# Performance work log

Hardware: AMD Instinct MI355X
Metric: run time of the kernel (lower is better)

Reference implementation:

```python
import jax, jax.numpy as jnp
import numpy as np

N_NODES = 50000
N_EDGES = 640000
DIM_IN = 128
DIM_OUT = 32
NUM_GRAPHS = 64


def setup_inputs() -> dict:
    key = jax.random.key(0)
    ks = jax.random.split(key, 8)
    x = jax.random.normal(ks[0], (N_NODES, DIM_IN), dtype=jnp.float32)
    edge_index = jax.random.randint(ks[1], (2, N_EDGES), 0, N_NODES, dtype=jnp.int64)
    batch = jnp.sort(jax.random.randint(ks[2], (N_NODES,), 0, NUM_GRAPHS, dtype=jnp.int64))
    s = 1.0 / np.sqrt(DIM_IN)
    W1 = jax.random.normal(ks[3], (DIM_IN, DIM_IN), dtype=jnp.float32) * s
    b1 = jnp.zeros((DIM_IN,), dtype=jnp.float32)
    W2 = jax.random.normal(ks[4], (DIM_IN, DIM_IN), dtype=jnp.float32) * s
    b2 = jnp.zeros((DIM_IN,), dtype=jnp.float32)
    Wh = jax.random.normal(ks[5], (DIM_IN, DIM_OUT), dtype=jnp.float32) * s
    bh = jnp.zeros((DIM_OUT,), dtype=jnp.float32)
    return {"x": x, "edge_index": edge_index, "batch": batch,
            "W1": W1, "b1": b1, "W2": W2, "b2": b2, "Wh": Wh, "bh": bh}


def _gcn_conv(x, src, dst, norm, W, b):
    # GCNConv: h = x @ W; out[i] = sum_{(j->i)} norm_e * h[j] + b
    h = x @ W
    msg = h[src] * norm[:, None]                      # [E+N, D] gather + scale
    out = jax.ops.segment_sum(msg, dst, num_segments=x.shape[0])
    return out + b


def reference(x, edge_index, batch, W1, b1, W2, b2, Wh, bh):
    n = x.shape[0]
    loops = jnp.arange(n, dtype=edge_index.dtype)
    src = jnp.concatenate([edge_index[0], loops])     # add self-loops
    dst = jnp.concatenate([edge_index[1], loops])
    # symmetric normalization: deg^{-1/2}[src] * deg^{-1/2}[dst]
    deg = jax.ops.segment_sum(jnp.ones_like(dst, dtype=x.dtype), dst, num_segments=n)
    dinv = jnp.where(deg > 0, jax.lax.rsqrt(deg), 0.0)
    norm = dinv[src] * dinv[dst]

    h = jax.nn.relu(_gcn_conv(x, src, dst, norm, W1, b1))   # dropout = identity (eval)
    h = jax.nn.relu(_gcn_conv(h, src, dst, norm, W2, b2))
    pooled = jax.ops.segment_sum(h, batch, num_segments=NUM_GRAPHS)  # global_add_pool
    logits = pooled @ Wh + bh
    return jax.nn.log_softmax(logits, axis=1)
```

## Files before the change

### kernel.cpp

```cpp
#include <hip/hip_runtime.h>
#include <hip/hip_bf16.h>
#include <math.h>

#define N_NODES 50000
#define N_EDGES 640000
#define DIM     128
#define NGRAPH  64
#define DOUT    32
#define CAP     64
#define LDSS 136
#define LDSF 132

#define G_GEMM  782
#define N_FILL  625
#define G_FRONT (G_GEMM + N_FILL)

#define G_PREP  209

typedef unsigned short u16;
typedef __attribute__((ext_vector_type(8))) short bf16x8;
typedef __attribute__((ext_vector_type(4))) float f32x4;

__device__ __forceinline__ u16 f2bf(float f) {
    unsigned u = __float_as_uint(f);
    return (u16)((u + 0x7FFFu + ((u >> 16) & 1u)) >> 16);
}
__device__ __forceinline__ float bf2f(u16 h) {
    return __uint_as_float(((unsigned)h) << 16);
}
__device__ __forceinline__ short2 cvt2(float x, float y) {
    __hip_bfloat162 h = __float22bfloat162_rn(make_float2(x, y));
    return *(short2*)&h;
}
__device__ __forceinline__ void upk(unsigned u, float& lo, float& hi) {
    lo = __uint_as_float(u << 16);
    hi = __uint_as_float(u & 0xFFFF0000u);
}

__global__ __launch_bounds__(256) void k_prep(const float* __restrict__ W1,
                                              const float* __restrict__ W2,
                                              u16* __restrict__ W1s,
                                              u16* __restrict__ W2s,
                                              float* __restrict__ pooled,
                                              int* __restrict__ cnt) {
    int b = blockIdx.x;
    int tid = threadIdx.x;
    if (b < 128) {
        int t = (b & 63) * 256 + tid;
        int j = t & 7, lane = (t >> 3) & 63, kc = (t >> 9) & 3, nt = t >> 11;
        int k = kc * 32 + (lane >> 4) * 8 + j;
        int n = nt * 16 + (lane & 15);
        if (b < 64) W1s[t] = f2bf(W1[k * 128 + n]);
        else        W2s[t] = f2bf(W2[k * 128 + n]);
    } else if (b < 160) {
        int t = (b - 128) * 256 + tid;
        pooled[t] = 0.f;
    } else {
        int t = (b - 160) * 256 + tid;
        if (t < 12500) {
            int4 z = {0, 0, 0, 0};
            *(int4*)(cnt + t * 4) = z;
        }
    }
}

__global__ __launch_bounds__(256) void k_front(const float* __restrict__ X,
                                               const int* __restrict__ src,
                                               const int* __restrict__ dst,
                                               int* __restrict__ cnt,
                                               int* __restrict__ bucket,
                                               const u16* __restrict__ Ws,
                                               u16* __restrict__ Y) {
    int b   = blockIdx.x;
    int tid = threadIdx.x;

    if (b < G_GEMM) {
        int wv   = tid >> 6;
        int lane = tid & 63;
        int row0 = b * 64 + wv * 16;
        int m    = lane & 15;
        int quad = lane >> 4;
        int ar = min(row0 + m, N_NODES - 1);
        const float* Arow = X + (size_t)ar * DIM;
        bf16x8 a[4];
#pragma unroll
        for (int kc = 0; kc < 4; ++kc) {
            const float4* p4 = (const float4*)(Arow + kc * 32 + quad * 8);
            float4 p = p4[0], q = p4[1];
            short2 s0 = cvt2(p.x, p.y), s1 = cvt2(p.z, p.w);
            short2 s2 = cvt2(q.x, q.y), s3 = cvt2(q.z, q.w);
            bf16x8 av;
            av[0] = s0.x; av[1] = s0.y; av[2] = s1.x; av[3] = s1.y;
            av[4] = s2.x; av[5] = s2.y; av[6] = s3.x; av[7] = s3.y;
            a[kc] = av;
        }
#pragma unroll
        for (int nt = 0; nt < 8; ++nt) {
            f32x4 acc = {0.f, 0.f, 0.f, 0.f};
#pragma unroll
            for (int kc = 0; kc < 4; ++kc) {
                bf16x8 bb = *(const bf16x8*)(Ws + ((size_t)(nt * 4 + kc) * 64 + lane) * 8);
                acc = __builtin_amdgcn_mfma_f32_16x16x32_bf16(a[kc], bb, acc, 0, 0, 0);
            }
            int col = nt * 16 + m;
#pragma unroll
            for (int r = 0; r < 4; ++r) {
                int rr = row0 + quad * 4 + r;
                if (rr < N_NODES) Y[(size_t)rr * DIM + col] = f2bf(acc[r]);
            }
        }
    } else {
        int e = (b - G_GEMM) * 1024 + tid * 4;
        int4 s4 = *(const int4*)(src + e);
        int4 d4 = *(const int4*)(dst + e);
        int p0 = atomicAdd(&cnt[d4.x], 1);
        int p1 = atomicAdd(&cnt[d4.y], 1);
        int p2 = atomicAdd(&cnt[d4.z], 1);
        int p3 = atomicAdd(&cnt[d4.w], 1);
        bucket[d4.x * CAP + p0] = s4.x;
        bucket[d4.y * CAP + p1] = s4.y;
        bucket[d4.z * CAP + p2] = s4.z;
        bucket[d4.w * CAP + p3] = s4.w;
    }
}

__global__ __launch_bounds__(256) void k_agg_gemm(const u16* __restrict__ H,
                                                  const int* __restrict__ bucket,
                                                  const int* __restrict__ cnt,
                                                  const float* __restrict__ bias,
                                                  const u16* __restrict__ Ws,
                                                  u16* __restrict__ Y) {
    __shared__ u16 As[16][LDSS];
    int tid    = threadIdx.x;
    int nloc   = tid >> 4;
    int lane16 = tid & 15;
    int node   = blockIdx.x * 16 + nloc;

    int deg = cnt[node];
    float dself = rsqrtf((float)(deg + 1));
    int e0 = node * CAP, e1 = e0 + deg;
    const uint4* H4 = (const uint4*)H;
    uint4 sv = H4[(size_t)node * 16 + lane16];
    float a0[8], a1[8] = {}, a2[8] = {}, a3[8] = {};
    {
        float lo, hi;
        upk(sv.x, lo, hi); a0[0] = dself * lo; a0[1] = dself * hi;
        upk(sv.y, lo, hi); a0[2] = dself * lo; a0[3] = dself * hi;
        upk(sv.z, lo, hi); a0[4] = dself * lo; a0[5] = dself * hi;
        upk(sv.w, lo, hi); a0[6] = dself * lo; a0[7] = dself * hi;
    }
    int4 c0, c1;
    if (e0 < e1) { c0 = *(const int4*)(bucket + e0); c1 = *(const int4*)(bucket + e0 + 4); }
    for (int e = e0; e < e1; e += 8) {
        int4 p0 = c0, p1 = c1;
        if (e + 8 < e1) {
            c0 = *(const int4*)(bucket + e + 8);
            c1 = *(const int4*)(bucket + e + 12);
        }
        int   idx[8];
        float w[8];
        uint4 v[8];
        int   cd[8];
        idx[0] = p0.x; idx[1] = p0.y; idx[2] = p0.z; idx[3] = p0.w;
        idx[4] = p1.x; idx[5] = p1.y; idx[6] = p1.z; idx[7] = p1.w;
#pragma unroll
        for (int u = 0; u < 8; ++u) {
            bool in = (e + u) < e1;
            w[u]   = in ? 1.f : 0.f;
            idx[u] = in ? idx[u] : 0;
        }
#pragma unroll
        for (int u = 0; u < 8; ++u) cd[u] = cnt[idx[u]];
#pragma unroll
        for (int u = 0; u < 8; ++u) v[u] = H4[(size_t)idx[u] * 16 + lane16];
#pragma unroll
        for (int u = 0; u < 8; ++u) w[u] *= rsqrtf((float)(cd[u] + 1));
#pragma unroll
        for (int u = 0; u < 8; ++u) {
            float* a = (u & 3) == 0 ? a0 : (u & 3) == 1 ? a1 : (u & 3) == 2 ? a2 : a3;
            float lo, hi;
            upk(v[u].x, lo, hi); a[0] = fmaf(w[u], lo, a[0]); a[1] = fmaf(w[u], hi, a[1]);
            upk(v[u].y, lo, hi); a[2] = fmaf(w[u], lo, a[2]); a[3] = fmaf(w[u], hi, a[3]);
            upk(v[u].z, lo, hi); a[4] = fmaf(w[u], lo, a[4]); a[5] = fmaf(w[u], hi, a[5]);
            upk(v[u].w, lo, hi); a[6] = fmaf(w[u], lo, a[6]); a[7] = fmaf(w[u], hi, a[7]);
        }
    }
    {
        float di = dself;
        const float4* b4 = (const float4*)bias;
        float4 blo = b4[lane16 * 2], bhi = b4[lane16 * 2 + 1];
        float r0 = fmaxf(di * (a0[0] + a1[0] + a2[0] + a3[0]) + blo.x, 0.f);
        float r1 = fmaxf(di * (a0[1] + a1[1] + a2[1] + a3[1]) + blo.y, 0.f);
        float r2 = fmaxf(di * (a0[2] + a1[2] + a2[2] + a3[2]) + blo.z, 0.f);
        float r3 = fmaxf(di * (a0[3] + a1[3] + a2[3] + a3[3]) + blo.w, 0.f);
        float r4 = fmaxf(di * (a0[4] + a1[4] + a2[4] + a3[4]) + bhi.x, 0.f);
        float r5 = fmaxf(di * (a0[5] + a1[5] + a2[5] + a3[5]) + bhi.y, 0.f);
        float r6 = fmaxf(di * (a0[6] + a1[6] + a2[6] + a3[6]) + bhi.z, 0.f);
        float r7 = fmaxf(di * (a0[7] + a1[7] + a2[7] + a3[7]) + bhi.w, 0.f);
        short2 s0 = cvt2(r0, r1), s1 = cvt2(r2, r3), s2 = cvt2(r4, r5), s3 = cvt2(r6, r7);
        uint4 o;
        o.x = *(unsigned*)&s0; o.y = *(unsigned*)&s1;
        o.z = *(unsigned*)&s2; o.w = *(unsigned*)&s3;
        *(uint4*)(&As[nloc][lane16 * 8]) = o;
    }
    __syncthreads();

    int wv   = tid >> 6;
    int lane = tid & 63;
    int m    = lane & 15;
    int quad = lane >> 4;
    bf16x8 a[4];
#pragma unroll
    for (int kc = 0; kc < 4; ++kc)
        a[kc] = *(const bf16x8*)(&As[m][kc * 32 + quad * 8]);
    float di[4];
#pragma unroll
    for (int r = 0; r < 4; ++r)
        di[r] = rsqrtf((float)(cnt[blockIdx.x * 16 + quad * 4 + r] + 1));
#pragma unroll
    for (int i = 0; i < 2; ++i) {
        int nt = wv * 2 + i;
        f32x4 acc = {0.f, 0.f, 0.f, 0.f};
#pragma unroll
        for (int kc = 0; kc < 4; ++kc) {
            bf16x8 b = *(const bf16x8*)(Ws + ((size_t)(nt * 4 + kc) * 64 + lane) * 8);
            acc = __builtin_amdgcn_mfma_f32_16x16x32_bf16(a[kc], b, acc, 0, 0, 0);
        }
        int col = nt * 16 + m;
#pragma unroll
        for (int r = 0; r < 4; ++r) {
            int rr = blockIdx.x * 16 + quad * 4 + r;
            Y[(size_t)rr * DIM + col] = f2bf(acc[r] * di[r]);
        }
    }
}

__global__ __launch_bounds__(256) void k_agg_pool(const u16* __restrict__ H,
                                                  const int* __restrict__ bucket,
                                                  const int* __restrict__ cnt,
                                                  const float* __restrict__ bias,
                                                  const int* __restrict__ batch,
                                                  float* __restrict__ pooled) {
    __shared__ float As[16][LDSF];
    __shared__ int bs[16];
    int tid  = threadIdx.x;
    int nloc = tid >> 4;
    int lane = tid & 15;
    int node = blockIdx.x * 16 + nloc;

    int deg = cnt[node];
    int e0 = node * CAP, e1 = e0 + deg;
    const uint4* H4 = (const uint4*)H;
    uint4 sv = H4[(size_t)node * 16 + lane];
    float a0[8], a1[8] = {}, a2[8] = {}, a3[8] = {};
    upk(sv.x, a0[0], a0[1]); upk(sv.y, a0[2], a0[3]);
    upk(sv.z, a0[4], a0[5]); upk(sv.w, a0[6], a0[7]);
    int4 c0, c1;
    if (e0 < e1) { c0 = *(const int4*)(bucket + e0); c1 = *(const int4*)(bucket + e0 + 4); }
    for (int e = e0; e < e1; e += 8) {
        int4 p0 = c0, p1 = c1;
        if (e + 8 < e1) {
            c0 = *(const int4*)(bucket + e + 8);
            c1 = *(const int4*)(bucket + e + 12);
        }
        int   idx[8];
        float w[8];
        uint4 v[8];
        idx[0] = p0.x; idx[1] = p0.y; idx[2] = p0.z; idx[3] = p0.w;
        idx[4] = p1.x; idx[5] = p1.y; idx[6] = p1.z; idx[7] = p1.w;
#pragma unroll
        for (int u = 0; u < 8; ++u) {
            bool in = (e + u) < e1;
            w[u]   = in ? 1.f : 0.f;
            idx[u] = in ? idx[u] : 0;
        }
#pragma unroll
        for (int u = 0; u < 8; ++u) v[u] = H4[(size_t)idx[u] * 16 + lane];
#pragma unroll
        for (int u = 0; u < 8; ++u) {
            float* a = (u & 3) == 0 ? a0 : (u & 3) == 1 ? a1 : (u & 3) == 2 ? a2 : a3;
            float lo, hi;
            upk(v[u].x, lo, hi); a[0] = fmaf(w[u], lo, a[0]); a[1] = fmaf(w[u], hi, a[1]);
            upk(v[u].y, lo, hi); a[2] = fmaf(w[u], lo, a[2]); a[3] = fmaf(w[u], hi, a[3]);
            upk(v[u].z, lo, hi); a[4] = fmaf(w[u], lo, a[4]); a[5] = fmaf(w[u], hi, a[5]);
            upk(v[u].w, lo, hi); a[6] = fmaf(w[u], lo, a[6]); a[7] = fmaf(w[u], hi, a[7]);
        }
    }
    {
        float di = rsqrtf((float)(deg + 1));
        const float4* b4 = (const float4*)bias;
        float4 blo = b4[lane * 2], bhi = b4[lane * 2 + 1];
        float4 olo, ohi;
        olo.x = fmaxf(di * (a0[0] + a1[0] + a2[0] + a3[0]) + blo.x, 0.f);
        olo.y = fmaxf(di * (a0[1] + a1[1] + a2[1] + a3[1]) + blo.y, 0.f);
        olo.z = fmaxf(di * (a0[2] + a1[2] + a2[2] + a3[2]) + blo.z, 0.f);
        olo.w = fmaxf(di * (a0[3] + a1[3] + a2[3] + a3[3]) + blo.w, 0.f);
        ohi.x = fmaxf(di * (a0[4] + a1[4] + a2[4] + a3[4]) + bhi.x, 0.f);
        ohi.y = fmaxf(di * (a0[5] + a1[5] + a2[5] + a3[5]) + bhi.y, 0.f);
        ohi.z = fmaxf(di * (a0[6] + a1[6] + a2[6] + a3[6]) + bhi.z, 0.f);
        ohi.w = fmaxf(di * (a0[7] + a1[7] + a2[7] + a3[7]) + bhi.w, 0.f);
        *(float4*)(&As[nloc][lane * 8])     = olo;
        *(float4*)(&As[nloc][lane * 8 + 4]) = ohi;
    }
    if (lane == 0) bs[nloc] = batch[node];
    __syncthreads();

    if (tid < 128) {
        float acc = 0.f;
        int cb = bs[0];
#pragma unroll
        for (int n = 0; n < 16; ++n) {
            int b = bs[n];
            if (b != cb) {
                atomicAdd(&pooled[cb * DIM + tid], acc);
                acc = 0.f; cb = b;
            }
            acc += As[n][tid];
        }
        atomicAdd(&pooled[cb * DIM + tid], acc);
    }
}

__global__ __launch_bounds__(64) void k_head(const float* __restrict__ pooled,
                                             const float* __restrict__ Wh,
                                             const float* __restrict__ bh,
                                             float* __restrict__ out) {
    int g = blockIdx.x;
    int lane = threadIdx.x;
    int c = lane & 31;
    const float* p = pooled + g * DIM;
    float lg = bh[c];
#pragma unroll 8
    for (int k = 0; k < DIM; ++k) lg = fmaf(p[k], Wh[k * DOUT + c], lg);
    float m = lg;
    for (int off = 16; off >= 1; off >>= 1) m = fmaxf(m, __shfl_xor(m, off, 32));
    float ex = expf(lg - m);
    float s = ex;
    for (int off = 16; off >= 1; off >>= 1) s += __shfl_xor(s, off, 32);
    if (lane < 32) out[g * DOUT + c] = lg - m - logf(s);
}

extern "C" void kernel_launch(void* const* d_in, const int* in_sizes, int n_in,
                              void* d_out, int out_size, void* d_ws, size_t ws_size,
                              hipStream_t stream) {
    const float* x     = (const float*)d_in[0];
    const int*   ei    = (const int*)d_in[1];
    const int*   batch = (const int*)d_in[2];
    const float* W1    = (const float*)d_in[3];
    const float* b1    = (const float*)d_in[4];
    const float* W2    = (const float*)d_in[5];
    const float* b2    = (const float*)d_in[6];
    const float* Wh    = (const float*)d_in[7];
    const float* bh    = (const float*)d_in[8];
    float* out = (float*)d_out;
    const int* src = ei;
    const int* dst = ei + N_EDGES;

    char* ws = (char*)d_ws;
    size_t off = 0;
    auto alloc = [&](size_t bytes) {
        void* p = ws + off;
        off += (bytes + 255) & ~(size_t)255;
        return p;
    };
    u16*   bufA   = (u16*) alloc((size_t)N_NODES * DIM * 2);
    u16*   bufB   = (u16*) alloc((size_t)N_NODES * DIM * 2);
    int*   cnt    = (int*) alloc((size_t)N_NODES * 4);
    int*   bucket = (int*) alloc((size_t)N_NODES * CAP * 4);
    u16*   W1s    = (u16*) alloc((size_t)DIM * DIM * 2);
    u16*   W2s    = (u16*) alloc((size_t)DIM * DIM * 2);
    float* pooled = (float*)alloc((size_t)NGRAPH * DIM * 4);
    (void)ws_size; (void)in_sizes; (void)n_in; (void)out_size;

    k_prep    <<<G_PREP, 256, 0, stream>>>(W1, W2, W1s, W2s, pooled, cnt);
    k_front   <<<G_FRONT, 256, 0, stream>>>(x, src, dst, cnt, bucket, W1s, bufA);
    k_agg_gemm<<<N_NODES / 16, 256, 0, stream>>>(bufA, bucket, cnt, b1, W2s, bufB);
    k_agg_pool<<<N_NODES / 16, 256, 0, stream>>>(bufB, bucket, cnt, b2, batch, pooled);

    k_head<<<NGRAPH, 64, 0, stream>>>(pooled, Wh, bh, out);
}
```

Measured before the change: 184.9 us.

## Replace fixed-capacity edge buckets with compact CSR built via degree count and scan

Degree counting moves into the prep kernel, and a single-block scan kernel computes padded per-node offsets, so edges are bucketed into a compact CSR-like array instead of a fixed 64-slot-per-node buffer. The goal is a smaller footprint and better locality for the bucket array, which the aggregation kernels read, and it removes the overflow risk of the fixed capacity. In exchange it adds a memset, an extra serial single-block scan launch, and a second round of atomics over all edges.

```diff
diff --git a/kernel.cpp b/kernel.cpp
--- a/kernel.cpp
+++ b/kernel.cpp
@@ -7,7 +7,6 @@
 #define DIM     128
 #define NGRAPH  64
 #define DOUT    32
-#define CAP     64
 #define LDSS 136
 #define LDSF 132
 
@@ -15,7 +14,7 @@
 #define N_FILL  625
 #define G_FRONT (G_GEMM + N_FILL)
 
-#define G_PREP  209
+#define G_PREP  785
 
 typedef unsigned short u16;
 typedef __attribute__((ext_vector_type(8))) short bf16x8;
@@ -39,6 +38,7 @@
 
 __global__ __launch_bounds__(256) void k_prep(const float* __restrict__ W1,
                                               const float* __restrict__ W2,
+                                              const int* __restrict__ dst,
                                               u16* __restrict__ W1s,
                                               u16* __restrict__ W2s,
                                               float* __restrict__ pooled,
@@ -56,10 +56,44 @@
         int t = (b - 128) * 256 + tid;
         pooled[t] = 0.f;
     } else {
-        int t = (b - 160) * 256 + tid;
-        if (t < 12500) {
-            int4 z = {0, 0, 0, 0};
-            *(int4*)(cnt + t * 4) = z;
+        int e = (b - 160) * 1024 + tid * 4;
+        int4 d4 = *(const int4*)(dst + e);
+        atomicAdd(&cnt[d4.x], 1);
+        atomicAdd(&cnt[d4.y], 1);
+        atomicAdd(&cnt[d4.z], 1);
+        atomicAdd(&cnt[d4.w], 1);
+    }
+}
+
+__global__ __launch_bounds__(1024) void k_scan(const int* __restrict__ cnt,
+                                               int* __restrict__ off,
+                                               int* __restrict__ woff) {
+    __shared__ int ls[1024];
+    int t = threadIdx.x;
+    int base = t * 49;
+    int s = 0;
+#pragma unroll 7
+    for (int k = 0; k < 49; ++k) {
+        int i = base + k;
+        if (i < N_NODES) s += (cnt[i] + 7) & ~7;
+    }
+    ls[t] = s;
+    __syncthreads();
+    for (int d = 1; d < 1024; d <<= 1) {
+        int v = 0;
+        if (t >= d) v = ls[t - d];
+        __syncthreads();
+        if (t >= d) ls[t] += v;
+        __syncthreads();
+    }
+    int run = ls[t] - s;
+#pragma unroll 7
+    for (int k = 0; k < 49; ++k) {
+        int i = base + k;
+        if (i < N_NODES) {
+            off[i]  = run;
+            woff[i] = run;
+            run += (cnt[i] + 7) & ~7;
         }
     }
 }
@@ -67,7 +101,7 @@
 __global__ __launch_bounds__(256) void k_front(const float* __restrict__ X,
                                                const int* __restrict__ src,
                                                const int* __restrict__ dst,
-                                               int* __restrict__ cnt,
+                                               int* __restrict__ woff,
                                                int* __restrict__ bucket,
                                                const u16* __restrict__ Ws,
                                                u16* __restrict__ Y) {
@@ -113,19 +147,20 @@
         int e = (b - G_GEMM) * 1024 + tid * 4;
         int4 s4 = *(const int4*)(src + e);
         int4 d4 = *(const int4*)(dst + e);
-        int p0 = atomicAdd(&cnt[d4.x], 1);
-        int p1 = atomicAdd(&cnt[d4.y], 1);
-        int p2 = atomicAdd(&cnt[d4.z], 1);
-        int p3 = atomicAdd(&cnt[d4.w], 1);
-        bucket[d4.x * CAP + p0] = s4.x;
-        bucket[d4.y * CAP + p1] = s4.y;
-        bucket[d4.z * CAP + p2] = s4.z;
-        bucket[d4.w * CAP + p3] = s4.w;
+        int p0 = atomicAdd(&woff[d4.x], 1);
+        int p1 = atomicAdd(&woff[d4.y], 1);
+        int p2 = atomicAdd(&woff[d4.z], 1);
+        int p3 = atomicAdd(&woff[d4.w], 1);
+        bucket[p0] = s4.x;
+        bucket[p1] = s4.y;
+        bucket[p2] = s4.z;
+        bucket[p3] = s4.w;
     }
 }
 
 __global__ __launch_bounds__(256) void k_agg_gemm(const u16* __restrict__ H,
                                                   const int* __restrict__ bucket,
+                                                  const int* __restrict__ off,
                                                   const int* __restrict__ cnt,
                                                   const float* __restrict__ bias,
                                                   const u16* __restrict__ Ws,
@@ -138,7 +173,7 @@
 
     int deg = cnt[node];
     float dself = rsqrtf((float)(deg + 1));
-    int e0 = node * CAP, e1 = e0 + deg;
+    int e0 = off[node], e1 = e0 + deg;
     const uint4* H4 = (const uint4*)H;
     uint4 sv = H4[(size_t)node * 16 + lane16];
     float a0[8], a1[8] = {}, a2[8] = {}, a3[8] = {};
@@ -237,6 +272,7 @@
 
 __global__ __launch_bounds__(256) void k_agg_pool(const u16* __restrict__ H,
                                                   const int* __restrict__ bucket,
+                                                  const int* __restrict__ off,
                                                   const int* __restrict__ cnt,
                                                   const float* __restrict__ bias,
                                                   const int* __restrict__ batch,
@@ -249,7 +285,7 @@
     int node = blockIdx.x * 16 + nloc;
 
     int deg = cnt[node];
-    int e0 = node * CAP, e1 = e0 + deg;
+    int e0 = off[node], e1 = e0 + deg;
     const uint4* H4 = (const uint4*)H;
     uint4 sv = H4[(size_t)node * 16 + lane];
     float a0[8], a1[8] = {}, a2[8] = {}, a3[8] = {};
@@ -357,25 +393,30 @@
     const int* dst = ei + N_EDGES;
 
     char* ws = (char*)d_ws;
-    size_t off = 0;
+    size_t woff_ = 0;
     auto alloc = [&](size_t bytes) {
-        void* p = ws + off;
-        off += (bytes + 255) & ~(size_t)255;
+        void* p = ws + woff_;
+        woff_ += (bytes + 255) & ~(size_t)255;
         return p;
     };
     u16*   bufA   = (u16*) alloc((size_t)N_NODES * DIM * 2);
     u16*   bufB   = (u16*) alloc((size_t)N_NODES * DIM * 2);
     int*   cnt    = (int*) alloc((size_t)N_NODES * 4);
-    int*   bucket = (int*) alloc((size_t)N_NODES * CAP * 4);
+    int*   off    = (int*) alloc((size_t)N_NODES * 4);
+    int*   woff   = (int*) alloc((size_t)N_NODES * 4);
+    int*   bucket = (int*) alloc((size_t)(N_EDGES + N_NODES * 8) * 4);
     u16*   W1s    = (u16*) alloc((size_t)DIM * DIM * 2);
     u16*   W2s    = (u16*) alloc((size_t)DIM * DIM * 2);
     float* pooled = (float*)alloc((size_t)NGRAPH * DIM * 4);
     (void)ws_size; (void)in_sizes; (void)n_in; (void)out_size;
 
-    k_prep    <<<G_PREP, 256, 0, stream>>>(W1, W2, W1s, W2s, pooled, cnt);
-    k_front   <<<G_FRONT, 256, 0, stream>>>(x, src, dst, cnt, bucket, W1s, bufA);
-    k_agg_gemm<<<N_NODES / 16, 256, 0, stream>>>(bufA, bucket, cnt, b1, W2s, bufB);
-    k_agg_pool<<<N_NODES / 16, 256, 0, stream>>>(bufB, bucket, cnt, b2, batch, pooled);
+    hipMemsetAsync(cnt, 0, (size_t)N_NODES * 4, stream);
+
+    k_prep    <<<G_PREP, 256, 0, stream>>>(W1, W2, dst, W1s, W2s, pooled, cnt);
+    k_scan    <<<1, 1024, 0, stream>>>(cnt, off, woff);
+    k_front   <<<G_FRONT, 256, 0, stream>>>(x, src, dst, woff, bucket, W1s, bufA);
+    k_agg_gemm<<<N_NODES / 16, 256, 0, stream>>>(bufA, bucket, off, cnt, b1, W2s, bufB);
+    k_agg_pool<<<N_NODES / 16, 256, 0, stream>>>(bufB, bucket, off, cnt, b2, batch, pooled);
 
     k_head<<<NGRAPH, 64, 0, stream>>>(pooled, Wh, bh, out);
 }
```

After: 341.0 us. 1.84x slower.
